# Kernel tuning notes

Hardware: AMD Instinct MI355X
Metric: run time of the kernel (lower is better)

Reference implementation:

```python
import jax, jax.numpy as jnp
import numpy as np

B, S, N, SD = 1024, 8, 64, 36
EPS = 1e-5

def _lrelu(x):
    return jnp.where(x > 0, x, 0.01 * x)

def _inorm(x, g, b):
    # x: [B,S,N,C]; InstanceNorm(axis=3) on a [1,1,N,C] tensor normalizes over N per channel
    mu = jnp.mean(x, axis=2, keepdims=True)
    var = jnp.var(x, axis=2, keepdims=True)
    return (x - mu) * jax.lax.rsqrt(var + EPS) * g + b

def _conv1d_same(x, w, b):
    # x: [B,S,Cin], w: [K,Cin,Cout]; TF 'same' even-kernel pads (0, k-1-pl)
    k = w.shape[0]
    pl = (k - 1) // 2
    y = jax.lax.conv_general_dilated(x, w, (1,), [(pl, k - 1 - pl)],
                                     dimension_numbers=('NWC', 'WIO', 'NWC'))
    return y + b

def setup_inputs() -> dict:
    key = jax.random.key(0)
    ks = iter(jax.random.split(key, 64))
    d = {}
    d['fts'] = jax.random.normal(next(ks), (B, S, N, 5), jnp.float32)
    d['state'] = jax.random.normal(next(ks), (B, S, SD), jnp.float32)
    def w(shape, scale=0.05):
        return jax.random.normal(next(ks), shape, jnp.float32) * scale
    # pointnet (1x1 Conv2D == pointwise matmul)
    d['pw1'] = w((5, 32)); d['pb1'] = jnp.zeros((32,)); d['pg1'] = jnp.ones((32,)); d['pbe1'] = jnp.zeros((32,))
    d['pw2'] = w((32, 64)); d['pb2'] = jnp.zeros((64,)); d['pg2'] = jnp.ones((64,)); d['pbe2'] = jnp.zeros((64,))
    d['pw3'] = w((64, 128)); d['pb3'] = jnp.zeros((128,)); d['pg3'] = jnp.ones((128,)); d['pbe3'] = jnp.zeros((128,))
    d['pw4'] = w((128, 128)); d['pb4'] = jnp.zeros((128,))
    # fts_mergenet Conv1D stack + Dense
    d['mw1'] = w((2, 128, 128)); d['mb1'] = jnp.zeros((128,))
    d['mw2'] = w((2, 128, 64)); d['mb2'] = jnp.zeros((64,))
    d['mw3'] = w((2, 64, 64)); d['mb3'] = jnp.zeros((64,))
    d['mw4'] = w((2, 64, 64)); d['mb4'] = jnp.zeros((64,))
    d['mdw'] = w((S * 64, 128)); d['mdb'] = jnp.zeros((128,))
    # states_conv Conv1D stack + Dense
    d['sw1'] = w((2, SD, 128)); d['sb1'] = jnp.zeros((128,))
    d['sw2'] = w((2, 128, 64)); d['sb2'] = jnp.zeros((64,))
    d['sw3'] = w((2, 64, 64)); d['sb3'] = jnp.zeros((64,))
    d['sw4'] = w((2, 64, 64)); d['sb4'] = jnp.zeros((64,))
    d['sdw'] = w((S * 64, 128)); d['sdb'] = jnp.zeros((128,))
    # control module Dense stack
    d['cw1'] = w((256, 128)); d['cb1'] = jnp.zeros((128,))
    d['cw2'] = w((128, 64)); d['cb2'] = jnp.zeros((64,))
    d['cw3'] = w((64, 32)); d['cb3'] = jnp.zeros((32,))
    d['cw4'] = w((32, 4)); d['cb4'] = jnp.zeros((4,))
    return d

def reference(fts, state, pw1, pb1, pg1, pbe1, pw2, pb2, pg2, pbe2,
              pw3, pb3, pg3, pbe3, pw4, pb4,
              mw1, mb1, mw2, mb2, mw3, mb3, mw4, mb4, mdw, mdb,
              sw1, sb1, sw2, sb2, sw3, sb3, sw4, sb4, sdw, sdb,
              cw1, cb1, cw2, cb2, cw3, cb3, cw4, cb4):
    # --- pointnet, fully batched over (B,S) instead of tf.map_fn per timestep ---
    x = fts  # [B,S,N,5]
    x = _lrelu(_inorm(jnp.einsum('bsnc,cd->bsnd', x, pw1) + pb1, pg1, pbe1))
    x = _lrelu(_inorm(jnp.einsum('bsnc,cd->bsnd', x, pw2) + pb2, pg2, pbe2))
    x = _lrelu(_inorm(jnp.einsum('bsnc,cd->bsnd', x, pw3) + pb3, pg3, pbe3))
    x = jnp.einsum('bsnc,cd->bsnd', x, pw4) + pb4
    emb = jnp.mean(x, axis=2)  # GlobalAveragePooling2D over (1,N) -> [B,S,128]
    # --- fts_mergenet ---
    y = _lrelu(_conv1d_same(emb, mw1, mb1))
    y = _lrelu(_conv1d_same(y, mw2, mb2))
    y = _lrelu(_conv1d_same(y, mw3, mb3))
    y = _lrelu(_conv1d_same(y, mw4, mb4))
    fts_emb = y.reshape(y.shape[0], -1) @ mdw + mdb  # [B,128]
    # --- states branch ---
    z = _lrelu(_conv1d_same(state, sw1, sb1))
    z = _lrelu(_conv1d_same(z, sw2, sb2))
    z = _lrelu(_conv1d_same(z, sw3, sb3))
    z = _conv1d_same(z, sw4, sb4)  # no activation after 4th conv
    st_emb = z.reshape(z.shape[0], -1) @ sdw + sdb  # [B,128]
    # --- control head ---
    t = jnp.concatenate([fts_emb, st_emb], axis=1)  # [B,256]
    t = _lrelu(t @ cw1 + cb1)
    t = _lrelu(t @ cw2 + cb2)
    t = _lrelu(t @ cw3 + cb3)
    out = t @ cw4 + cb4  # [B,4]
    thrust = jax.nn.sigmoid(out[:, :1])
    body = jnp.tanh(out[:, 1:])
    mult = jnp.array([21.0, 6.0, 6.0, 6.0], dtype=out.dtype)
    return jnp.concatenate([thrust, body], axis=1) * mult
```

## Files before the change

### kernel.cpp

```cpp
#include <hip/hip_runtime.h>
#include <hip/hip_bf16.h>
#include <math.h>

#define THREADS 256

constexpr int S   = 8;
constexpr int NPT = 64;
constexpr int SD  = 36;
constexpr float EPS = 1e-5f;

constexpr int NPREP = 119;

typedef float v4f __attribute__((ext_vector_type(4)));
typedef __attribute__((ext_vector_type(8))) short bf8;
typedef __attribute__((ext_vector_type(4))) float f4;

__device__ __forceinline__ float lrelu(float x) { return fmaxf(x, 0.01f * x); }

__device__ __forceinline__ unsigned short f2bf(float x) {
  return __builtin_bit_cast(unsigned short, __float2bfloat16(x));
}

__device__ __forceinline__ void pack_frag(const float* __restrict__ src, unsigned short* __restrict__ dst,
                                          int slot, int NT, int TS, int CIN, int N) {
  const int f = slot >> 6, l = slot & 63;
  const int nt = f % NT, kt = f / NT;
  const int n = nt * 16 + (l & 15), g = (l >> 4);
  unsigned short* d = dst + (size_t)f * 512 + l * 8;
#pragma unroll
  for (int j = 0; j < 8; ++j) {
    int k = kt * 32 + g * 8 + j;
    float v;
    if (TS > 0) { int tap = k / TS, c = k - tap * TS; v = (c < CIN) ? src[(tap * CIN + c) * N + n] : 0.f; }
    else        v = (CIN == 0 || k < CIN) ? src[k * N + n] : 0.f;
    d[j] = f2bf(v);
  }
}

__device__ __forceinline__ void pack_frag_fold(const float* __restrict__ pw4,
    const float* __restrict__ mw1, unsigned short* __restrict__ dst, int slot) {
  const int f = slot >> 6, l = slot & 63;
  const int nt = f & 7, kt = f >> 3;
  const int n = nt * 16 + (l & 15), g = l >> 4;
  const int k0 = kt * 32 + g * 8;
  const int tap = k0 >> 7, c0 = k0 & 127;
  const float* mcol = mw1 + (size_t)tap * 128 * 128 + n;
  unsigned short* dd = dst + (size_t)f * 512 + l * 8;
#pragma unroll 1
  for (int half = 0; half < 2; ++half) {
    float acc[4] = {};
    const float* pbase = pw4 + (size_t)(c0 + half * 4) * 128;
#pragma unroll 1
    for (int d4 = 0; d4 < 32; ++d4) {
      const int d0 = 4 * d4;
      float m0 = mcol[(size_t)(d0 + 0) * 128];
      float m1 = mcol[(size_t)(d0 + 1) * 128];
      float m2 = mcol[(size_t)(d0 + 2) * 128];
      float m3 = mcol[(size_t)(d0 + 3) * 128];
#pragma unroll
      for (int j = 0; j < 4; ++j) {
        v4f pv = *(const v4f*)(pbase + j * 128 + d0);
        acc[j] = fmaf(pv[0], m0, fmaf(pv[1], m1, fmaf(pv[2], m2, fmaf(pv[3], m3, acc[j]))));
      }
    }
#pragma unroll
    for (int j = 0; j < 4; ++j) dd[half * 4 + j] = f2bf(acc[j]);
  }
}

#define WOFF_PNW1 0
#define WOFF_PNW2 1024
#define WOFF_PNW3 3072
#define WOFF_MW1  11264
#define WOFF_MW2  44032
#define WOFF_MW3  60416
#define WOFF_MW4  68608
#define WOFF_MDW  76800
#define WOFF_SW1  142336
#define WOFF_SW2  154624
#define WOFF_SW3  171008
#define WOFF_SW4  179200
#define WOFF_SDW  187392

__global__ void prep_pn(const float* __restrict__ pw1, const float* __restrict__ pw2,
                        const float* __restrict__ pw3, unsigned short* __restrict__ wf) {
  const int slot = blockIdx.x * 256 + threadIdx.x;
  if      (slot <  128) pack_frag(pw1, wf + WOFF_PNW1, slot,       2, 0,   5,  32);
  else if (slot <  384) pack_frag(pw2, wf + WOFF_PNW2, slot - 128, 4, 0,   0,  64);
  else if (slot < 1408) pack_frag(pw3, wf + WOFF_PNW3, slot - 384, 8, 0,   0, 128);
}

__device__ __forceinline__ void pack_tail_slot(int slot,
    const float* __restrict__ pw4, const float* __restrict__ pb4,
    const float* __restrict__ mw1, const float* __restrict__ mb1,
    const float* __restrict__ mw2, const float* __restrict__ mw3,
    const float* __restrict__ mw4, const float* __restrict__ mdw,
    const float* __restrict__ sw1, const float* __restrict__ sw2, const float* __restrict__ sw3,
    const float* __restrict__ sw4, const float* __restrict__ sdw,
    unsigned short* __restrict__ wf, float* __restrict__ mb1p, float* __restrict__ mb1p7) {
  if      (slot <  5504) pack_frag_fold(pw4, mw1, wf + WOFF_MW1, slot - 1408);
  else if (slot <  7552) pack_frag(mw2,    wf + WOFF_MW2,  slot - 5504,   4, 128, 128,  64);
  else if (slot <  8576) pack_frag(mw3,    wf + WOFF_MW3,  slot - 7552,   4,  64,  64,  64);
  else if (slot <  9600) pack_frag(mw4,    wf + WOFF_MW4,  slot - 8576,   4,  64,  64,  64);
  else if (slot < 17792) pack_frag(mdw,    wf + WOFF_MDW,  slot - 9600,   8,   0,   0, 128);
  else if (slot < 19328) pack_frag(sw1,    wf + WOFF_SW1,  slot - 17792,  8,  48,  36, 128);
  else if (slot < 21376) pack_frag(sw2,    wf + WOFF_SW2,  slot - 19328,  4, 128, 128,  64);
  else if (slot < 22400) pack_frag(sw3,    wf + WOFF_SW3,  slot - 21376,  4,  64,  64,  64);
  else if (slot < 23424) pack_frag(sw4,    wf + WOFF_SW4,  slot - 22400,  4,  64,  64,  64);
  else if (slot < 31616) pack_frag(sdw,    wf + WOFF_SDW,  slot - 23424,  8,   0,   0, 128);
  else if (slot < 31744) {
    const int n = slot - 31616;
    float a = mb1[n];
#pragma unroll 1
    for (int d = 0; d < 128; ++d)
      a = fmaf(pb4[d], mw1[(size_t)d * 128 + n] + mw1[(size_t)(128 + d) * 128 + n], a);
    mb1p[n] = a;
  } else if (slot < 31872) {
    const int n = slot - 31744;
    float a = mb1[n];
#pragma unroll 1
    for (int d = 0; d < 128; ++d) a = fmaf(pb4[d], mw1[(size_t)d * 128 + n], a);
    mb1p7[n] = a;
  }
}

__global__ __launch_bounds__(THREADS)
void pointnet_kernel(const float* __restrict__ fts,
    const unsigned short* __restrict__ wf,
    const float* __restrict__ pg1, const float* __restrict__ pbe1,
    const float* __restrict__ pg2, const float* __restrict__ pbe2,
    const float* __restrict__ pg3, const float* __restrict__ pbe3,
    const float* __restrict__ pw4, const float* __restrict__ pb4,
    const float* __restrict__ mw1, const float* __restrict__ mb1,
    const float* __restrict__ mw2, const float* __restrict__ mw3,
    const float* __restrict__ mw4, const float* __restrict__ mdw,
    const float* __restrict__ sw1, const float* __restrict__ sw2, const float* __restrict__ sw3,
    const float* __restrict__ sw4, const float* __restrict__ sdw,
    unsigned short* __restrict__ wf_out, float* __restrict__ mb1p, float* __restrict__ mb1p7,
    unsigned short* __restrict__ xbar_out)
{
  if (blockIdx.x < NPREP) {
    pack_tail_slot(blockIdx.x * 256 + threadIdx.x + 1408,
                   pw4, pb4, mw1, mb1, mw2, mw3, mw4, mdw,
                   sw1, sw2, sw3, sw4, sdw, wf_out, mb1p, mb1p7);
    return;
  }
  const int p = blockIdx.x - NPREP;
  const int t = threadIdx.x;
  const int l = t & 63, w = t >> 6;
  const int g = l >> 4, lc = l & 15;
  const unsigned short* w1f = wf + WOFF_PNW1;
  const unsigned short* w2f = wf + WOFF_PNW2;
  const unsigned short* w3f = wf + WOFF_PNW3;

  __shared__ unsigned short xinb[64 * 40];
  __shared__ unsigned short x1b[64 * 40];
  __shared__ unsigned short x2b[64 * 72];

  {
    const float* src = fts + (size_t)p * 320;
    unsigned* xz = (unsigned*)xinb;
    const int row = t >> 2, cp = t & 3;
    const float* sr = src + row * 5;
    unsigned v0 = 0u;
    if (cp == 0)      v0 = (unsigned)f2bf(sr[0]) | ((unsigned)f2bf(sr[1]) << 16);
    else if (cp == 1) v0 = (unsigned)f2bf(sr[2]) | ((unsigned)f2bf(sr[3]) << 16);
    else if (cp == 2) v0 = (unsigned)f2bf(sr[4]);
    unsigned* xr = xz + row * 20;
    xr[cp]      = v0;
    xr[cp + 4]  = 0u;
    xr[cp + 8]  = 0u;
    xr[cp + 12] = 0u;
  }
  __syncthreads();

  if (w < 2) {
    f4 c1[4];
#pragma unroll
    for (int mt = 0; mt < 4; ++mt) c1[mt] = f4{0.f, 0.f, 0.f, 0.f};
    bf8 bfrag = *(const bf8*)(w1f + ((size_t)w * 64 + l) * 8);
#pragma unroll
    for (int mt = 0; mt < 4; ++mt) {
      bf8 afrag = *(const bf8*)(xinb + (mt * 16 + lc) * 40 + g * 8);
      c1[mt] = __builtin_amdgcn_mfma_f32_16x16x32_bf16(afrag, bfrag, c1[mt], 0, 0, 0);
    }
    float s = 0.f, q = 0.f;
#pragma unroll
    for (int mt = 0; mt < 4; ++mt)
#pragma unroll
      for (int r = 0; r < 4; ++r) { float v = c1[mt][r]; s += v; q = fmaf(v, v, q); }
    s += __shfl_xor(s, 16, 64); s += __shfl_xor(s, 32, 64);
    q += __shfl_xor(q, 16, 64); q += __shfl_xor(q, 32, 64);
    const int ch = w * 16 + lc;
    float mu  = s * (1.f / NPT);
    float inv = rsqrtf(q * (1.f / NPT) - mu * mu + EPS);
    float a = inv * pg1[ch];
    float bb = fmaf(-mu, a, pbe1[ch]);
#pragma unroll
    for (int mt = 0; mt < 4; ++mt)
#pragma unroll
      for (int r = 0; r < 4; ++r) {
        int row = mt * 16 + g * 4 + r;
        x1b[row * 40 + ch] = f2bf(lrelu(fmaf(c1[mt][r], a, bb)));
      }
  }
  __syncthreads();

  f4 c2[4];
#pragma unroll
  for (int mt = 0; mt < 4; ++mt) c2[mt] = f4{0.f, 0.f, 0.f, 0.f};
  {
    bf8 bfrag = *(const bf8*)(w2f + ((size_t)w * 64 + l) * 8);
#pragma unroll
    for (int mt = 0; mt < 4; ++mt) {
      bf8 afrag = *(const bf8*)(x1b + (mt * 16 + lc) * 40 + g * 8);
      c2[mt] = __builtin_amdgcn_mfma_f32_16x16x32_bf16(afrag, bfrag, c2[mt], 0, 0, 0);
    }
  }
  {
    float s = 0.f, q = 0.f;
#pragma unroll
    for (int mt = 0; mt < 4; ++mt)
#pragma unroll
      for (int r = 0; r < 4; ++r) { float v = c2[mt][r]; s += v; q = fmaf(v, v, q); }
    s += __shfl_xor(s, 16, 64); s += __shfl_xor(s, 32, 64);
    q += __shfl_xor(q, 16, 64); q += __shfl_xor(q, 32, 64);
    const int ch = w * 16 + lc;
    float mu  = s * (1.f / NPT);
    float inv = rsqrtf(q * (1.f / NPT) - mu * mu + EPS);
    float a = inv * pg2[ch];
    float bb = fmaf(-mu, a, pbe2[ch]);
#pragma unroll
    for (int mt = 0; mt < 4; ++mt)
#pragma unroll
      for (int r = 0; r < 4; ++r) {
        int row = mt * 16 + g * 4 + r;
        x2b[row * 72 + ch] = f2bf(lrelu(fmaf(c2[mt][r], a, bb)));
      }
  }
  __syncthreads();

  f4 c3[4][2];
#pragma unroll
  for (int mt = 0; mt < 4; ++mt)
#pragma unroll
    for (int n = 0; n < 2; ++n) c3[mt][n] = f4{0.f, 0.f, 0.f, 0.f};
  bf8 bf3[2][2];
#pragma unroll
  for (int ntl = 0; ntl < 2; ++ntl)
#pragma unroll
    for (int kt = 0; kt < 2; ++kt)
      bf3[ntl][kt] = *(const bf8*)(w3f + ((size_t)(kt * 8 + (2 * w + ntl)) * 64 + l) * 8);
#pragma unroll
  for (int mt = 0; mt < 4; ++mt)
#pragma unroll
    for (int kt = 0; kt < 2; ++kt) {
      bf8 afrag = *(const bf8*)(x2b + (mt * 16 + lc) * 72 + kt * 32 + g * 8);
#pragma unroll
      for (int ntl = 0; ntl < 2; ++ntl)
        c3[mt][ntl] = __builtin_amdgcn_mfma_f32_16x16x32_bf16(afrag, bf3[ntl][kt], c3[mt][ntl], 0, 0, 0);
    }

#pragma unroll
  for (int ntl = 0; ntl < 2; ++ntl) {
    float s = 0.f, q = 0.f;
#pragma unroll
    for (int mt = 0; mt < 4; ++mt)
#pragma unroll
      for (int r = 0; r < 4; ++r) { float v = c3[mt][ntl][r]; s += v; q = fmaf(v, v, q); }
    s += __shfl_xor(s, 16, 64); s += __shfl_xor(s, 32, 64);
    q += __shfl_xor(q, 16, 64); q += __shfl_xor(q, 32, 64);
    const int ch = w * 32 + ntl * 16 + lc;
    float mu  = s * (1.f / NPT);
    float inv = rsqrtf(q * (1.f / NPT) - mu * mu + EPS);
    float a = inv * pg3[ch];
    float bb = fmaf(-mu, a, pbe3[ch]);
    float m = 0.f;
#pragma unroll
    for (int mt = 0; mt < 4; ++mt)
#pragma unroll
      for (int r = 0; r < 4; ++r) m += lrelu(fmaf(c3[mt][ntl][r], a, bb));
    m += __shfl_xor(m, 16, 64); m += __shfl_xor(m, 32, 64);
    if (g == 0) xbar_out[(size_t)p * 128 + ch] = f2bf(m * (1.f / NPT));
  }
}

template<int KT, int NT, int TS, int SPI, int SPO, bool ACT>
__device__ __forceinline__ void mfma_conv(const unsigned short* __restrict__ xin,
    unsigned short* __restrict__ xout, const unsigned short* __restrict__ wfr,
    const float* __restrict__ bias, const float* __restrict__ bias7, int w, int l) {
  const int g = l >> 4, lc = l & 15;
  const int arow = w * 16 + lc, abl = arow >> 3, an = arow & 7;
  f4 acc[NT];
#pragma unroll
  for (int nt = 0; nt < NT; ++nt) acc[nt] = f4{0.f, 0.f, 0.f, 0.f};
#pragma unroll
  for (int kt = 0; kt < KT; ++kt) {
    const int k0 = kt * 32 + g * 8;
    const int tap = k0 / TS, c = k0 - tap * TS;
    bf8 a = *(const bf8*)(xin + (abl * 9 + an + tap) * SPI + c);
#pragma unroll
    for (int nt = 0; nt < NT; ++nt) {
      bf8 b = *(const bf8*)(wfr + ((size_t)(kt * NT + nt) * 64 + l) * 8);
      acc[nt] = __builtin_amdgcn_mfma_f32_16x16x32_bf16(a, b, acc[nt], 0, 0, 0);
    }
  }
  const int orow0 = w * 16 + g * 4;
#pragma unroll
  for (int nt = 0; nt < NT; ++nt) {
    const float bv  = bias[nt * 16 + lc];
    const float bv7 = bias7[nt * 16 + lc];
#pragma unroll
    for (int r = 0; r < 4; ++r) {
      const int rr = orow0 + r, obl = rr >> 3, on = rr & 7;
      float v = acc[nt][r] + (on == 7 ? bv7 : bv);
      if (ACT) v = lrelu(v);
      xout[(obl * 9 + on) * SPO + nt * 16 + lc] = f2bf(v);
    }
  }
}

__device__ __forceinline__ void mfma_dense512(const unsigned short* __restrict__ xin,
    float* __restrict__ P, const unsigned short* __restrict__ wfr, int w, int l) {
  const int g = l >> 4, lc = l & 15;
  const int bl = lc & 7;
  f4 acc[8];
#pragma unroll
  for (int nt = 0; nt < 8; ++nt) acc[nt] = f4{0.f, 0.f, 0.f, 0.f};
#pragma unroll
  for (int kt2 = 0; kt2 < 4; ++kt2) {
    const int kt = w * 4 + kt2;
    const int k0 = kt * 32 + g * 8;
    const int n = k0 >> 6, c = k0 & 63;
    bf8 a = *(const bf8*)(xin + (bl * 9 + n) * 72 + c);
#pragma unroll
    for (int nt = 0; nt < 8; ++nt) {
      bf8 b = *(const bf8*)(wfr + ((size_t)(kt * 8 + nt) * 64 + l) * 8);
      acc[nt] = __builtin_amdgcn_mfma_f32_16x16x32_bf16(a, b, acc[nt], 0, 0, 0);
    }
  }
  if (g < 2) {
#pragma unroll
    for (int nt = 0; nt < 8; ++nt)
#pragma unroll
      for (int r = 0; r < 4; ++r) {
        const int rr = g * 4 + r;
        P[(w * 8 + rr) * 128 + nt * 16 + lc] = acc[nt][r];
      }
  }
}

__global__ __launch_bounds__(THREADS)
void tail_mfma_kernel(const unsigned short* __restrict__ xbar, const float* __restrict__ state,
    const unsigned short* __restrict__ wf,
    const float* __restrict__ mb1p, const float* __restrict__ mb1p7,
    const float* __restrict__ mb2, const float* __restrict__ mb3,
    const float* __restrict__ mb4, const float* __restrict__ mdb,
    const float* __restrict__ sb1, const float* __restrict__ sb2, const float* __restrict__ sb3,
    const float* __restrict__ sb4, const float* __restrict__ sdb,
    float* __restrict__ femb, float* __restrict__ semb)
{
  const int t = threadIdx.x, l = t & 63, w = t >> 6;
  const bool merge = blockIdx.x < 128;
  const int bg = merge ? blockIdx.x : blockIdx.x - 128;

  __shared__ unsigned short lds[24768];
  unsigned short* BufX = lds;
  unsigned short* BufY = lds + 9792;
  unsigned short* BufZ = lds + 19584;

  { unsigned* z = (unsigned*)BufX; for (int i = t; i < 4896; i += THREADS) z[i] = 0; }
  for (int i = t; i < 8 * 136; i += THREADS) BufY[((i / 136) * 9 + 8) * 136 + (i % 136)] = 0;
  for (int i = t; i < 8 * 72;  i += THREADS) BufZ[((i / 72)  * 9 + 8) * 72  + (i % 72)]  = 0;

  if (merge) {
    for (int i = t; i < 1024; i += THREADS) {
      int bl = i >> 7, rem = i & 127, n = rem >> 4, sl = rem & 15;
      bf8 v = *(const bf8*)(xbar + (size_t)((bg * 8 + bl) * 8 + n) * 128 + sl * 8);
      *(bf8*)(BufX + (bl * 9 + n) * 136 + sl * 8) = v;
    }
  } else {
    for (int i = t; i < 2304; i += THREADS) {
      int bl = i / 288, rem = i % 288, n = rem / 36, c = rem % 36;
      BufX[(bl * 9 + n) * 48 + c] = f2bf(state[((size_t)(bg * 8 + bl) * 8 + n) * 36 + c]);
    }
  }
  __syncthreads();

  if (merge) mfma_conv<8, 8, 128, 136, 136, true>(BufX, BufY, wf + WOFF_MW1, mb1p, mb1p7, w, l);
  else       mfma_conv<3, 8,  48,  48, 136, true>(BufX, BufY, wf + WOFF_SW1, sb1, sb1, w, l);
  __syncthreads();
  if (merge) mfma_conv<8, 4, 128, 136, 72, true>(BufY, BufZ, wf + WOFF_MW2, mb2, mb2, w, l);
  else       mfma_conv<8, 4, 128, 136, 72, true>(BufY, BufZ, wf + WOFF_SW2, sb2, sb2, w, l);
  __syncthreads();
  for (int i = t; i < 8 * 72; i += THREADS) BufX[((i / 72) * 9 + 8) * 72 + (i % 72)] = 0;
  __syncthreads();
  if (merge) mfma_conv<4, 4, 64, 72, 72, true>(BufZ, BufX, wf + WOFF_MW3, mb3, mb3, w, l);
  else       mfma_conv<4, 4, 64, 72, 72, true>(BufZ, BufX, wf + WOFF_SW3, sb3, sb3, w, l);
  __syncthreads();
  if (merge) mfma_conv<4, 4, 64, 72, 72, true >(BufX, BufY, wf + WOFF_MW4, mb4, mb4, w, l);
  else       mfma_conv<4, 4, 64, 72, 72, false>(BufX, BufY, wf + WOFF_SW4, sb4, sb4, w, l);
  __syncthreads();

  float* P = (float*)lds;
  mfma_dense512(BufY, P, wf + (merge ? WOFF_MDW : WOFF_SDW), w, l);
  __syncthreads();

  const float* bias = merge ? mdb : sdb;
  float* outg = (merge ? femb : semb) + (size_t)bg * 1024;
  for (int i = t; i < 1024; i += THREADS) {
    int ch = i & 127, b = i >> 7;
    outg[i] = bias[ch] + P[(0 * 8 + b) * 128 + ch] + P[(1 * 8 + b) * 128 + ch]
                       + P[(2 * 8 + b) * 128 + ch] + P[(3 * 8 + b) * 128 + ch];
  }
}

template<int CIN, int COUT, bool ACT>
__device__ __forceinline__ void wave_dense(const float* __restrict__ in, float* __restrict__ out,
                                           const float* __restrict__ W, const float* __restrict__ bias, int l) {
  if constexpr (COUT >= 64) {
    constexpr int NC = COUT / 64;
    const int d0 = l * NC;
    float acc[NC];
#pragma unroll
    for (int k = 0; k < NC; ++k) acc[k] = bias[d0 + k];
#pragma unroll 4
    for (int c4 = 0; c4 < CIN / 4; ++c4) {
      v4f x4 = *(const v4f*)(in + 4 * c4);
#pragma unroll
      for (int j = 0; j < 4; ++j) {
        const float* wr = W + (4 * c4 + j) * COUT + d0;
#pragma unroll
        for (int k = 0; k < NC; ++k) acc[k] = fmaf(x4[j], wr[k], acc[k]);
      }
    }
#pragma unroll
    for (int k = 0; k < NC; ++k) out[d0 + k] = ACT ? lrelu(acc[k]) : acc[k];
  } else {
    if (l < COUT) {
      float acc = bias[l];
#pragma unroll 4
      for (int c4 = 0; c4 < CIN / 4; ++c4) {
        v4f x4 = *(const v4f*)(in + 4 * c4);
#pragma unroll
        for (int j = 0; j < 4; ++j) acc = fmaf(x4[j], W[(4 * c4 + j) * COUT + l], acc);
      }
      out[l] = ACT ? lrelu(acc) : acc;
    }
  }
}

__global__ __launch_bounds__(THREADS)
void head_kernel(const float* __restrict__ femb, const float* __restrict__ semb,
    const float* __restrict__ cw1, const float* __restrict__ cb1,
    const float* __restrict__ cw2, const float* __restrict__ cb2,
    const float* __restrict__ cw3, const float* __restrict__ cb3,
    const float* __restrict__ cw4, const float* __restrict__ cb4,
    float* __restrict__ out)
{
  const int t = threadIdx.x, l = t & 63, w = t >> 6;
  const int b = blockIdx.x * 4 + w;
  __shared__ float cat[4][256];
  __shared__ float hb[4][232];

  {
    v4f v;
    if (l < 32) v = *(const v4f*)(femb + (size_t)b * 128 + 4 * l);
    else        v = *(const v4f*)(semb + (size_t)b * 128 + 4 * (l - 32));
    *(v4f*)(&cat[w][4 * l]) = v;
  }
  wave_dense<256, 128, true>(cat[w], hb[w], cw1, cb1, l);
  wave_dense<128, 64, true>(hb[w], hb[w] + 128, cw2, cb2, l);
  wave_dense<64, 32, true>(hb[w] + 128, hb[w] + 192, cw3, cb3, l);
  if (l < 4) {
    float acc = cb4[l];
#pragma unroll
    for (int c = 0; c < 32; ++c) acc = fmaf(hb[w][192 + c], cw4[c * 4 + l], acc);
    out[(size_t)b * 4 + l] = (l == 0) ? 21.f / (1.f + expf(-acc)) : 6.f * tanhf(acc);
  }
}

extern "C" void kernel_launch(void* const* d_in, const int* in_sizes, int n_in,
                              void* d_out, int out_size, void* d_ws, size_t ws_size,
                              hipStream_t stream) {
  const float* p[44];
  for (int i = 0; i < 44; ++i) p[i] = (const float*)d_in[i];

  unsigned short* xbar_bf = (unsigned short*)d_ws;
  float* femb  = (float*)((char*)d_ws + 2097152);
  float* semb  = (float*)((char*)d_ws + 2621440);
  unsigned short* wf = (unsigned short*)((char*)d_ws + 3145728);
  float* mb1p  = (float*)((char*)d_ws + 3651584);
  float* mb1p7 = (float*)((char*)d_ws + 3652096);

  prep_pn<<<6, THREADS, 0, stream>>>(p[2], p[6], p[10], wf);

  pointnet_kernel<<<NPREP + 1024 * S, THREADS, 0, stream>>>(
      p[0], wf,
      p[4], p[5], p[8], p[9], p[12], p[13],
      p[14], p[15], p[16], p[17],
      p[18], p[20], p[22], p[24],
      p[26], p[28], p[30], p[32], p[34],
      wf, mb1p, mb1p7,
      xbar_bf);

  tail_mfma_kernel<<<256, THREADS, 0, stream>>>(
      xbar_bf, p[1], wf,
      mb1p, mb1p7, p[19], p[21], p[23], p[25],
      p[27], p[29], p[31], p[33], p[35],
      femb, semb);

  head_kernel<<<256, THREADS, 0, stream>>>(
      femb, semb,
      p[36], p[37], p[38], p[39], p[40], p[41], p[42], p[43],
      (float*)d_out);
}
```

Baseline: 72.34 us.

## Halve batch per tail block and split conv tiles across 2x2 wave grid

The tail kernel now handles 4 batch items per block instead of 8 and launches 512 blocks instead of 256. Conv MFMA work is split across a 2x2 wave arrangement: two waves cover the rows and each wave computes half the output column tiles. The dense512 stage uses half of the MFMA rows. LDS use per block is halved. The aim is to fill more CUs on a 256-CU part, at the cost of redundant weight loads across more blocks and wasted MFMA rows in the dense stage.

```diff
diff --git a/kernel.cpp b/kernel.cpp
--- a/kernel.cpp
+++ b/kernel.cpp
@@ -286,44 +286,47 @@
 }
 
 template<int KT, int NT, int TS, int SPI, int SPO, bool ACT>
-__device__ __forceinline__ void mfma_conv(const unsigned short* __restrict__ xin,
+__device__ __forceinline__ void mfma_conv4(const unsigned short* __restrict__ xin,
     unsigned short* __restrict__ xout, const unsigned short* __restrict__ wfr,
-    const float* __restrict__ bias, const float* __restrict__ bias7, int w, int l) {
+    const float* __restrict__ bias, const float* __restrict__ bias7, int wm, int wn, int l) {
   const int g = l >> 4, lc = l & 15;
-  const int arow = w * 16 + lc, abl = arow >> 3, an = arow & 7;
-  f4 acc[NT];
-#pragma unroll
-  for (int nt = 0; nt < NT; ++nt) acc[nt] = f4{0.f, 0.f, 0.f, 0.f};
+  const int arow = wm * 16 + lc, abl = arow >> 3, an = arow & 7;
+  constexpr int NTH = NT / 2;
+  f4 acc[NTH];
+#pragma unroll
+  for (int nth = 0; nth < NTH; ++nth) acc[nth] = f4{0.f, 0.f, 0.f, 0.f};
 #pragma unroll
   for (int kt = 0; kt < KT; ++kt) {
     const int k0 = kt * 32 + g * 8;
     const int tap = k0 / TS, c = k0 - tap * TS;
     bf8 a = *(const bf8*)(xin + (abl * 9 + an + tap) * SPI + c);
 #pragma unroll
-    for (int nt = 0; nt < NT; ++nt) {
+    for (int nth = 0; nth < NTH; ++nth) {
+      const int nt = wn * NTH + nth;
       bf8 b = *(const bf8*)(wfr + ((size_t)(kt * NT + nt) * 64 + l) * 8);
-      acc[nt] = __builtin_amdgcn_mfma_f32_16x16x32_bf16(a, b, acc[nt], 0, 0, 0);
-    }
-  }
-  const int orow0 = w * 16 + g * 4;
-#pragma unroll
-  for (int nt = 0; nt < NT; ++nt) {
+      acc[nth] = __builtin_amdgcn_mfma_f32_16x16x32_bf16(a, b, acc[nth], 0, 0, 0);
+    }
+  }
+  const int orow0 = wm * 16 + g * 4;
+#pragma unroll
+  for (int nth = 0; nth < NTH; ++nth) {
+    const int nt = wn * NTH + nth;
     const float bv  = bias[nt * 16 + lc];
     const float bv7 = bias7[nt * 16 + lc];
 #pragma unroll
     for (int r = 0; r < 4; ++r) {
       const int rr = orow0 + r, obl = rr >> 3, on = rr & 7;
-      float v = acc[nt][r] + (on == 7 ? bv7 : bv);
+      float v = acc[nth][r] + (on == 7 ? bv7 : bv);
       if (ACT) v = lrelu(v);
       xout[(obl * 9 + on) * SPO + nt * 16 + lc] = f2bf(v);
     }
   }
 }
 
-__device__ __forceinline__ void mfma_dense512(const unsigned short* __restrict__ xin,
+__device__ __forceinline__ void mfma_dense512_g4(const unsigned short* __restrict__ xin,
     float* __restrict__ P, const unsigned short* __restrict__ wfr, int w, int l) {
   const int g = l >> 4, lc = l & 15;
-  const int bl = lc & 7;
+  const int bl = lc & 3;
   f4 acc[8];
 #pragma unroll
   for (int nt = 0; nt < 8; ++nt) acc[nt] = f4{0.f, 0.f, 0.f, 0.f};
@@ -339,14 +342,12 @@
       acc[nt] = __builtin_amdgcn_mfma_f32_16x16x32_bf16(a, b, acc[nt], 0, 0, 0);
     }
   }
-  if (g < 2) {
+  if (g == 0) {
 #pragma unroll
     for (int nt = 0; nt < 8; ++nt)
 #pragma unroll
-      for (int r = 0; r < 4; ++r) {
-        const int rr = g * 4 + r;
-        P[(w * 8 + rr) * 128 + nt * 16 + lc] = acc[nt][r];
-      }
+      for (int r = 0; r < 4; ++r)
+        P[(w * 4 + r) * 128 + nt * 16 + lc] = acc[nt][r];
   }
 }
 
@@ -361,57 +362,58 @@
     float* __restrict__ femb, float* __restrict__ semb)
 {
   const int t = threadIdx.x, l = t & 63, w = t >> 6;
-  const bool merge = blockIdx.x < 128;
-  const int bg = merge ? blockIdx.x : blockIdx.x - 128;
-
-  __shared__ unsigned short lds[24768];
+  const int wm = w >> 1, wn = w & 1;
+  const bool merge = blockIdx.x < 256;
+  const int bg = merge ? blockIdx.x : blockIdx.x - 256;
+
+  __shared__ unsigned short lds[12384];
   unsigned short* BufX = lds;
-  unsigned short* BufY = lds + 9792;
-  unsigned short* BufZ = lds + 19584;
-
-  { unsigned* z = (unsigned*)BufX; for (int i = t; i < 4896; i += THREADS) z[i] = 0; }
-  for (int i = t; i < 8 * 136; i += THREADS) BufY[((i / 136) * 9 + 8) * 136 + (i % 136)] = 0;
-  for (int i = t; i < 8 * 72;  i += THREADS) BufZ[((i / 72)  * 9 + 8) * 72  + (i % 72)]  = 0;
+  unsigned short* BufY = lds + 4896;
+  unsigned short* BufZ = lds + 9792;
+
+  { unsigned* z = (unsigned*)BufX; for (int i = t; i < 2448; i += THREADS) z[i] = 0; }
+  for (int i = t; i < 4 * 136; i += THREADS) BufY[((i / 136) * 9 + 8) * 136 + (i % 136)] = 0;
+  if (t < 4 * 72) BufZ[((t / 72) * 9 + 8) * 72 + (t % 72)] = 0;
 
   if (merge) {
-    for (int i = t; i < 1024; i += THREADS) {
+    for (int i = t; i < 512; i += THREADS) {
       int bl = i >> 7, rem = i & 127, n = rem >> 4, sl = rem & 15;
-      bf8 v = *(const bf8*)(xbar + (size_t)((bg * 8 + bl) * 8 + n) * 128 + sl * 8);
+      bf8 v = *(const bf8*)(xbar + (size_t)((bg * 4 + bl) * 8 + n) * 128 + sl * 8);
       *(bf8*)(BufX + (bl * 9 + n) * 136 + sl * 8) = v;
     }
   } else {
-    for (int i = t; i < 2304; i += THREADS) {
+    for (int i = t; i < 1152; i += THREADS) {
       int bl = i / 288, rem = i % 288, n = rem / 36, c = rem % 36;
-      BufX[(bl * 9 + n) * 48 + c] = f2bf(state[((size_t)(bg * 8 + bl) * 8 + n) * 36 + c]);
-    }
-  }
-  __syncthreads();
-
-  if (merge) mfma_conv<8, 8, 128, 136, 136, true>(BufX, BufY, wf + WOFF_MW1, mb1p, mb1p7, w, l);
-  else       mfma_conv<3, 8,  48,  48, 136, true>(BufX, BufY, wf + WOFF_SW1, sb1, sb1, w, l);
-  __syncthreads();
-  if (merge) mfma_conv<8, 4, 128, 136, 72, true>(BufY, BufZ, wf + WOFF_MW2, mb2, mb2, w, l);
-  else       mfma_conv<8, 4, 128, 136, 72, true>(BufY, BufZ, wf + WOFF_SW2, sb2, sb2, w, l);
-  __syncthreads();
-  for (int i = t; i < 8 * 72; i += THREADS) BufX[((i / 72) * 9 + 8) * 72 + (i % 72)] = 0;
-  __syncthreads();
-  if (merge) mfma_conv<4, 4, 64, 72, 72, true>(BufZ, BufX, wf + WOFF_MW3, mb3, mb3, w, l);
-  else       mfma_conv<4, 4, 64, 72, 72, true>(BufZ, BufX, wf + WOFF_SW3, sb3, sb3, w, l);
-  __syncthreads();
-  if (merge) mfma_conv<4, 4, 64, 72, 72, true >(BufX, BufY, wf + WOFF_MW4, mb4, mb4, w, l);
-  else       mfma_conv<4, 4, 64, 72, 72, false>(BufX, BufY, wf + WOFF_SW4, sb4, sb4, w, l);
+      BufX[(bl * 9 + n) * 48 + c] = f2bf(state[((size_t)(bg * 4 + bl) * 8 + n) * 36 + c]);
+    }
+  }
+  __syncthreads();
+
+  if (merge) mfma_conv4<8, 8, 128, 136, 136, true>(BufX, BufY, wf + WOFF_MW1, mb1p, mb1p7, wm, wn, l);
+  else       mfma_conv4<3, 8,  48,  48, 136, true>(BufX, BufY, wf + WOFF_SW1, sb1, sb1, wm, wn, l);
+  __syncthreads();
+  if (merge) mfma_conv4<8, 4, 128, 136, 72, true>(BufY, BufZ, wf + WOFF_MW2, mb2, mb2, wm, wn, l);
+  else       mfma_conv4<8, 4, 128, 136, 72, true>(BufY, BufZ, wf + WOFF_SW2, sb2, sb2, wm, wn, l);
+  __syncthreads();
+  if (t < 4 * 72) BufX[((t / 72) * 9 + 8) * 72 + (t % 72)] = 0;
+  __syncthreads();
+  if (merge) mfma_conv4<4, 4, 64, 72, 72, true>(BufZ, BufX, wf + WOFF_MW3, mb3, mb3, wm, wn, l);
+  else       mfma_conv4<4, 4, 64, 72, 72, true>(BufZ, BufX, wf + WOFF_SW3, sb3, sb3, wm, wn, l);
+  __syncthreads();
+  if (merge) mfma_conv4<4, 4, 64, 72, 72, true >(BufX, BufY, wf + WOFF_MW4, mb4, mb4, wm, wn, l);
+  else       mfma_conv4<4, 4, 64, 72, 72, false>(BufX, BufY, wf + WOFF_SW4, sb4, sb4, wm, wn, l);
   __syncthreads();
 
   float* P = (float*)lds;
-  mfma_dense512(BufY, P, wf + (merge ? WOFF_MDW : WOFF_SDW), w, l);
+  mfma_dense512_g4(BufY, P, wf + (merge ? WOFF_MDW : WOFF_SDW), w, l);
   __syncthreads();
 
   const float* bias = merge ? mdb : sdb;
-  float* outg = (merge ? femb : semb) + (size_t)bg * 1024;
-  for (int i = t; i < 1024; i += THREADS) {
+  float* outg = (merge ? femb : semb) + (size_t)bg * 512;
+  for (int i = t; i < 512; i += THREADS) {
     int ch = i & 127, b = i >> 7;
-    outg[i] = bias[ch] + P[(0 * 8 + b) * 128 + ch] + P[(1 * 8 + b) * 128 + ch]
-                       + P[(2 * 8 + b) * 128 + ch] + P[(3 * 8 + b) * 128 + ch];
+    outg[i] = bias[ch] + P[(0 + b) * 128 + ch] + P[(4 + b) * 128 + ch]
+                       + P[(8 + b) * 128 + ch] + P[(12 + b) * 128 + ch];
   }
 }
 
@@ -504,7 +506,7 @@
       wf, mb1p, mb1p7,
       xbar_bf);
 
-  tail_mfma_kernel<<<256, THREADS, 0, stream>>>(
+  tail_mfma_kernel<<<512, THREADS, 0, stream>>>(
       xbar_bf, p[1], wf,
       mb1p, mb1p7, p[19], p[21], p[23], p[25],
       p[27], p[29], p[31], p[33], p[35],
```

Result: faster. 68.61 us (-5.2%).
